# Kernel tuning notes

Measured on AMD Instinct MI355X. Metric: run time of the kernel, lower is better.

The kernel has to match this reference:

```python
import jax, jax.numpy as jnp
import numpy as np

N, E, IN, HID, HEADS, OUT = 20000, 320000, 64, 32, 8, 128
EPS_SM = 1e-16


def setup_inputs() -> dict:
    key = jax.random.key(0)
    ks = iter(jax.random.split(key, 40))
    def g(shape, scale=0.1):
        return jax.random.normal(next(ks), shape, dtype=jnp.float32) * scale
    inp = {
        "x": jax.random.normal(next(ks), (N, IN), dtype=jnp.float32),
        "edge_index": jax.random.randint(next(ks), (2, E), 0, N, dtype=jnp.int64),
        # layer 0: GATConv(64 -> 32, heads=8, concat) => dim 256
        "W0": g((IN, HEADS * HID)), "b0": jnp.zeros((HEADS * HID,), jnp.float32),
        "as0": g((HEADS, HID)), "ad0": g((HEADS, HID)),
        "lng0": jnp.ones((HEADS * HID,), jnp.float32), "lnb0": jnp.zeros((HEADS * HID,), jnp.float32),
        "rW0": g((IN, HEADS * HID)), "rb0": jnp.zeros((HEADS * HID,), jnp.float32),
        "rw0": jnp.ones((1,), jnp.float32),
        # layer 1: GATConv(256 -> 32, heads=8, concat) => dim 256, residual = Identity
        "W1": g((HEADS * HID, HEADS * HID)), "b1": jnp.zeros((HEADS * HID,), jnp.float32),
        "as1": g((HEADS, HID)), "ad1": g((HEADS, HID)),
        "lng1": jnp.ones((HEADS * HID,), jnp.float32), "lnb1": jnp.zeros((HEADS * HID,), jnp.float32),
        "rw1": jnp.ones((1,), jnp.float32),
        # layer 2: GATConv(256 -> 128, heads=8, concat=False mean) => dim 128
        "W2": g((HEADS * HID, HEADS * OUT)), "b2": jnp.zeros((OUT,), jnp.float32),
        "as2": g((HEADS, OUT)), "ad2": g((HEADS, OUT)),
        "lng2": jnp.ones((OUT,), jnp.float32), "lnb2": jnp.zeros((OUT,), jnp.float32),
        "rW2": g((HEADS * HID, OUT)), "rb2": jnp.zeros((OUT,), jnp.float32),
        "rw2": jnp.ones((1,), jnp.float32),
    }
    return inp


def _gat_conv(x, src, dst, W, b, a_s, a_d, heads, out_c, concat):
    n = x.shape[0]
    h = (x @ W).reshape(n, heads, out_c)            # [N,H,C]
    al_s = jnp.sum(h * a_s, axis=-1)                 # [N,H]
    al_d = jnp.sum(h * a_d, axis=-1)
    e = jax.nn.leaky_relu(al_s[src] + al_d[dst], 0.2)  # [E,H]
    m = jax.ops.segment_max(e, dst, num_segments=n)
    m = jnp.where(jnp.isfinite(m), m, 0.0)
    ex = jnp.exp(e - m[dst])
    denom = jax.ops.segment_sum(ex, dst, num_segments=n)
    alpha = ex / (denom[dst] + EPS_SM)               # [E,H]
    msg = alpha[:, :, None] * h[src]                 # [E,H,C]
    out = jax.ops.segment_sum(msg, dst, num_segments=n)  # [N,H,C]
    if concat:
        return out.reshape(n, heads * out_c) + b
    return out.mean(axis=1) + b


def _layer_norm(x, g, b, eps=1e-5):
    mu = x.mean(-1, keepdims=True)
    var = x.var(-1, keepdims=True)
    return (x - mu) * jax.lax.rsqrt(var + eps) * g + b


def reference(x, edge_index, W0, b0, as0, ad0, lng0, lnb0, rW0, rb0, rw0,
              W1, b1, as1, ad1, lng1, lnb1, rw1,
              W2, b2, as2, ad2, lng2, lnb2, rW2, rb2, rw2):
    ei = edge_index.astype(jnp.int32)
    ar = jnp.arange(N, dtype=jnp.int32)
    src = jnp.concatenate([ei[0], ar])               # add self loops
    dst = jnp.concatenate([ei[1], ar])

    # layer 0 (eval mode: dropout is identity)
    g0 = _gat_conv(x, src, dst, W0, b0, as0, ad0, HEADS, HID, True)
    h = _layer_norm(g0, lng0, lnb0) + jax.nn.sigmoid(rw0) * (x @ rW0 + rb0)
    h = jax.nn.elu(h)

    # layer 1 (residual projection = Identity)
    g1 = _gat_conv(h, src, dst, W1, b1, as1, ad1, HEADS, HID, True)
    h = jax.nn.elu(_layer_norm(g1, lng1, lnb1) + jax.nn.sigmoid(rw1) * h)

    # layer 2 (concat=False -> mean over heads)
    g2 = _gat_conv(h, src, dst, W2, b2, as2, ad2, HEADS, OUT, False)
    out = _layer_norm(g2, lng2, lnb2) + jax.nn.sigmoid(rw2) * (h @ rW2 + rb2)
    return out
```

## Files before the change

kernel.cpp:

```cpp
#include <hip/hip_runtime.h>
#include <cstddef>
#include <cstdint>

#define NN 20000
#define EE 320000
#define ET (EE + NN)

typedef __attribute__((ext_vector_type(8))) short bf16x8;
typedef __attribute__((ext_vector_type(4))) float f32x4;

__device__ __forceinline__ unsigned short f2bf_rne(float f) {
  unsigned int u = __float_as_uint(f);
  u += 0x7FFF + ((u >> 16) & 1);
  return (unsigned short)(u >> 16);
}

__device__ __forceinline__ float bf2f(unsigned short b) {
  return __uint_as_float(((unsigned int)b) << 16);
}

__device__ __forceinline__ f32x4 up2(uint2 p) {
  f32x4 v = {__uint_as_float(p.x << 16), __uint_as_float(p.x & 0xFFFF0000u),
             __uint_as_float(p.y << 16), __uint_as_float(p.y & 0xFFFF0000u)};
  return v;
}


__global__ __launch_bounds__(256) void prep_all(
    const float* __restrict__ x, unsigned short* __restrict__ xbf,
    const float* __restrict__ W0, unsigned short* __restrict__ W0T,
    const float* __restrict__ rW0, unsigned short* __restrict__ rW0T,
    const float* __restrict__ W1, unsigned short* __restrict__ W1T,
    const float* __restrict__ rW2, unsigned short* __restrict__ rW2T,
    const float* __restrict__ W2, const float* __restrict__ as2,
    const float* __restrict__ ad2, unsigned short* __restrict__ V16,
    unsigned short* __restrict__ WstkT, int* __restrict__ zbuf, int full) {
  int b = blockIdx.x, t = threadIdx.x;
  if (b < 5000) {
    int i = b * 256 + t;
    if (i < NN * 64) xbf[i] = f2bf_rne(x[i]);
    return;
  }
  b -= 5000;
  if (b < 64) {
    int idx = b * 256 + t, n = idx >> 6, k = idx & 63;
    W0T[idx] = f2bf_rne(W0[(size_t)k * 256 + n]);
    return;
  }
  b -= 64;
  if (b < 64) {
    int idx = b * 256 + t, n = idx >> 6, k = idx & 63;
    rW0T[idx] = f2bf_rne(rW0[(size_t)k * 256 + n]);
    return;
  }
  b -= 64;
  if (b < 256) {
    int idx = b * 256 + t, n = idx >> 8, k = idx & 255;
    W1T[idx] = f2bf_rne(W1[(size_t)k * 256 + n]);
    return;
  }
  b -= 256;
  if (b < 128) {
    int idx = b * 256 + t, n = idx >> 8, k = idx & 255;
    rW2T[idx] = f2bf_rne(rW2[(size_t)k * 128 + n]);
    return;
  }
  b -= 128;
  if (b < 157) {
    int i = b * 256 + t;
    if (i < 2 * NN) zbuf[i] = 0;
    return;
  }
  b -= 157;
  if (!full) return;
  if (b < 16) {
    int r = b, k = t, h = r & 7;
    const float* av = (r < 8) ? (as2 + h * 128) : (ad2 + h * 128);
    const float* wr = W2 + (size_t)k * 1024 + h * 128;
    float v = 0.f;
#pragma unroll 4
    for (int c = 0; c < 128; ++c) v += wr[c] * av[c];
    V16[(size_t)r * 256 + k] = f2bf_rne(v);
    return;
  }
  b -= 16;
  if (b < 128) {
    int c = b, k = t;
#pragma unroll
    for (int h = 0; h < 8; ++h)
      WstkT[(size_t)c * 2048 + h * 256 + k] =
          f2bf_rne(0.125f * W2[(size_t)k * 1024 + h * 128 + c]);
  }
}

#define PREP_BLOCKS (5000 + 64 + 64 + 256 + 128 + 157 + 16 + 128)


__global__ __launch_bounds__(256) void zero_f32(float* __restrict__ p, int n) {
  int i = blockIdx.x * 256 + threadIdx.x;
  if (i < n) p[i] = 0.f;
}

__global__ void tconv(const float* __restrict__ src, unsigned short* __restrict__ dst,
                      int N) {
  int n = blockIdx.x, k = threadIdx.x, K = blockDim.x;
  dst[(size_t)n * K + k] = f2bf_rne(src[(size_t)k * N + n]);
}


__global__ __launch_bounds__(256) void count_kernel(const int* __restrict__ ei,
                                                    int* __restrict__ deg) {
  int e = blockIdx.x * 256 + threadIdx.x;
  if (e < EE) {
    int d = ei[EE + e];
    if (d >= 0 && d < NN) atomicAdd(&deg[d], 1);
  }
}

__global__ __launch_bounds__(1024) void scan_blk(const int* __restrict__ deg,
    int* __restrict__ offs, int* __restrict__ bsum) {
  __shared__ int s[1024];
  int b = blockIdx.x, tid = threadIdx.x;
  int i = b * 1024 + tid;
  s[tid] = (i < NN) ? (deg[i] + 1) : 0;
  __syncthreads();
  for (int off = 1; off < 1024; off <<= 1) {
    int t = (tid >= off) ? s[tid - off] : 0;
    __syncthreads();
    s[tid] += t;
    __syncthreads();
  }
  if (i < NN) offs[i + 1] = s[tid];
  if (tid == 1023) bsum[b] = s[1023];
}

__global__ __launch_bounds__(256) void scan_add(int* __restrict__ offs,
    const int* __restrict__ bsum) {
  int i = blockIdx.x * 256 + threadIdx.x;
  if (i == 0) offs[0] = 0;
  if (i < NN) {
    int b = i >> 10;
    int pre = 0;
    for (int k = 0; k < b; ++k) pre += bsum[k];
    offs[i + 1] += pre;
  }
}

__global__ __launch_bounds__(256) void scatter_kernel(const int* __restrict__ ei,
    const int* __restrict__ offs, int* __restrict__ cursor, int* __restrict__ csr) {
  int e = blockIdx.x * 256 + threadIdx.x;
  if (e >= ET) return;
  int s, d;
  if (e < EE) { s = ei[e]; d = ei[EE + e]; }
  else        { s = e - EE; d = s; }
  if (s < 0 || s >= NN || d < 0 || d >= NN) return;
  int pos = atomicAdd(&cursor[d], 1);
  csr[offs[d] + pos] = s;
}


__global__ __launch_bounds__(256) void gemm_mfma(const unsigned short* __restrict__ A,
    const unsigned short* __restrict__ BT, const float* __restrict__ bias,
    float* __restrict__ C, int M, int K, int ldc) {
  int bm = blockIdx.y * 64, bn = blockIdx.x * 64;
  int tid = threadIdx.x;
  int w = tid >> 6, l = tid & 63;
  int wm = bm + w * 16;
  if (wm >= M) return;
  int lane16 = l & 15, q = l >> 4;
  const unsigned short* ap = A + (size_t)(wm + lane16) * K + q * 8;
  const unsigned short* bp = BT + (size_t)(bn + lane16) * K + q * 8;
  f32x4 acc0 = {0.f, 0.f, 0.f, 0.f}, acc1 = acc0, acc2 = acc0, acc3 = acc0;
#pragma unroll 2
  for (int k0 = 0; k0 < K; k0 += 32) {
    bf16x8 a  = *(const bf16x8*)(ap + k0);
    bf16x8 b0 = *(const bf16x8*)(bp + k0);
    bf16x8 b1 = *(const bf16x8*)(bp + (size_t)16 * K + k0);
    bf16x8 b2 = *(const bf16x8*)(bp + (size_t)32 * K + k0);
    bf16x8 b3 = *(const bf16x8*)(bp + (size_t)48 * K + k0);
    acc0 = __builtin_amdgcn_mfma_f32_16x16x32_bf16(a, b0, acc0, 0, 0, 0);
    acc1 = __builtin_amdgcn_mfma_f32_16x16x32_bf16(a, b1, acc1, 0, 0, 0);
    acc2 = __builtin_amdgcn_mfma_f32_16x16x32_bf16(a, b2, acc2, 0, 0, 0);
    acc3 = __builtin_amdgcn_mfma_f32_16x16x32_bf16(a, b3, acc3, 0, 0, 0);
  }
  int row0 = wm + q * 4;
  int c0 = bn + lane16;
  float bi0 = bias ? bias[c0]      : 0.f;
  float bi1 = bias ? bias[c0 + 16] : 0.f;
  float bi2 = bias ? bias[c0 + 32] : 0.f;
  float bi3 = bias ? bias[c0 + 48] : 0.f;
#pragma unroll
  for (int r = 0; r < 4; ++r) {
    float* crow = C + (size_t)(row0 + r) * ldc;
    crow[c0]      = acc0[r] + bi0;
    crow[c0 + 16] = acc1[r] + bi1;
    crow[c0 + 32] = acc2[r] + bi2;
    crow[c0 + 48] = acc3[r] + bi3;
  }
}

__global__ __launch_bounds__(256) void gemm_l0(const unsigned short* __restrict__ A,
    const unsigned short* __restrict__ W0T, const unsigned short* __restrict__ rW0T,
    const float* __restrict__ rb0, unsigned short* __restrict__ hG,
    unsigned short* __restrict__ resout, const float* __restrict__ as_w,
    const float* __restrict__ ad_w, float* __restrict__ als,
    float* __restrict__ ald, int M) {
  int z = blockIdx.z;
  int bm = blockIdx.y * 64, bn = blockIdx.x * 64;
  int tid = threadIdx.x;
  int w = tid >> 6, l = tid & 63;
  int wm = bm + w * 16;
  if (wm >= M) return;
  int lane16 = l & 15, q = l >> 4;
  const unsigned short* BT = z ? rW0T : W0T;
  const unsigned short* ap = A + (size_t)(wm + lane16) * 64 + q * 8;
  const unsigned short* bp = BT + (size_t)(bn + lane16) * 64 + q * 8;
  f32x4 acc0 = {0.f, 0.f, 0.f, 0.f}, acc1 = acc0, acc2 = acc0, acc3 = acc0;
#pragma unroll
  for (int k0 = 0; k0 < 64; k0 += 32) {
    bf16x8 a  = *(const bf16x8*)(ap + k0);
    bf16x8 b0 = *(const bf16x8*)(bp + k0);
    bf16x8 b1 = *(const bf16x8*)(bp + (size_t)16 * 64 + k0);
    bf16x8 b2 = *(const bf16x8*)(bp + (size_t)32 * 64 + k0);
    bf16x8 b3 = *(const bf16x8*)(bp + (size_t)48 * 64 + k0);
    acc0 = __builtin_amdgcn_mfma_f32_16x16x32_bf16(a, b0, acc0, 0, 0, 0);
    acc1 = __builtin_amdgcn_mfma_f32_16x16x32_bf16(a, b1, acc1, 0, 0, 0);
    acc2 = __builtin_amdgcn_mfma_f32_16x16x32_bf16(a, b2, acc2, 0, 0, 0);
    acc3 = __builtin_amdgcn_mfma_f32_16x16x32_bf16(a, b3, acc3, 0, 0, 0);
  }
  int row0 = wm + q * 4;
  int c0 = bn + lane16;
  if (z == 1) {
    float bi0 = rb0[c0], bi1 = rb0[c0 + 16], bi2 = rb0[c0 + 32], bi3 = rb0[c0 + 48];
#pragma unroll
    for (int r = 0; r < 4; ++r) {
      unsigned short* crow = resout + (size_t)(row0 + r) * 256;
      crow[c0]      = f2bf_rne(acc0[r] + bi0);
      crow[c0 + 16] = f2bf_rne(acc1[r] + bi1);
      crow[c0 + 32] = f2bf_rne(acc2[r] + bi2);
      crow[c0 + 48] = f2bf_rne(acc3[r] + bi3);
    }
    return;
  }
#pragma unroll
  for (int r = 0; r < 4; ++r) {
    unsigned short* crow = hG + (size_t)(row0 + r) * 256;
    crow[c0]      = f2bf_rne(acc0[r]);
    crow[c0 + 16] = f2bf_rne(acc1[r]);
    crow[c0 + 32] = f2bf_rne(acc2[r]);
    crow[c0 + 48] = f2bf_rne(acc3[r]);
  }
  float asA0 = as_w[c0],      asA1 = as_w[c0 + 16];
  float adA0 = ad_w[c0],      adA1 = ad_w[c0 + 16];
  float asB0 = as_w[c0 + 32], asB1 = as_w[c0 + 48];
  float adB0 = ad_w[c0 + 32], adB1 = ad_w[c0 + 48];
  int hA = (bn >> 5), hB = hA + 1;
#pragma unroll
  for (int r = 0; r < 4; ++r) {
    float sA = acc0[r] * asA0 + acc1[r] * asA1;
    float dA = acc0[r] * adA0 + acc1[r] * adA1;
    float sB = acc2[r] * asB0 + acc3[r] * asB1;
    float dB = acc2[r] * adB0 + acc3[r] * adB1;
#pragma unroll
    for (int off = 8; off >= 1; off >>= 1) {
      sA += __shfl_xor(sA, off);
      dA += __shfl_xor(dA, off);
      sB += __shfl_xor(sB, off);
      dB += __shfl_xor(dB, off);
    }
    if (lane16 == 0) {
      int row = row0 + r;
      als[row * 8 + hA] = sA;
      ald[row * 8 + hA] = dA;
      als[row * 8 + hB] = sB;
      ald[row * 8 + hB] = dB;
    }
  }
}

__global__ __launch_bounds__(256) void gemm_mfma_bf_al(const unsigned short* __restrict__ A,
    const unsigned short* __restrict__ BT, unsigned short* __restrict__ C,
    const float* __restrict__ as_w, const float* __restrict__ ad_w,
    float* __restrict__ als, float* __restrict__ ald, int M, int K) {
  int bm = blockIdx.y * 64, bn = blockIdx.x * 64;
  int tid = threadIdx.x;
  int w = tid >> 6, l = tid & 63;
  int wm = bm + w * 16;
  if (wm >= M) return;
  int lane16 = l & 15, q = l >> 4;
  const unsigned short* ap = A + (size_t)(wm + lane16) * K + q * 8;
  const unsigned short* bp = BT + (size_t)(bn + lane16) * K + q * 8;
  f32x4 acc0 = {0.f, 0.f, 0.f, 0.f}, acc1 = acc0, acc2 = acc0, acc3 = acc0;
#pragma unroll 2
  for (int k0 = 0; k0 < K; k0 += 32) {
    bf16x8 a  = *(const bf16x8*)(ap + k0);
    bf16x8 b0 = *(const bf16x8*)(bp + k0);
    bf16x8 b1 = *(const bf16x8*)(bp + (size_t)16 * K + k0);
    bf16x8 b2 = *(const bf16x8*)(bp + (size_t)32 * K + k0);
    bf16x8 b3 = *(const bf16x8*)(bp + (size_t)48 * K + k0);
    acc0 = __builtin_amdgcn_mfma_f32_16x16x32_bf16(a, b0, acc0, 0, 0, 0);
    acc1 = __builtin_amdgcn_mfma_f32_16x16x32_bf16(a, b1, acc1, 0, 0, 0);
    acc2 = __builtin_amdgcn_mfma_f32_16x16x32_bf16(a, b2, acc2, 0, 0, 0);
    acc3 = __builtin_amdgcn_mfma_f32_16x16x32_bf16(a, b3, acc3, 0, 0, 0);
  }
  int row0 = wm + q * 4;
  int c0 = bn + lane16;
#pragma unroll
  for (int r = 0; r < 4; ++r) {
    unsigned short* crow = C + (size_t)(row0 + r) * 256;
    crow[c0]      = f2bf_rne(acc0[r]);
    crow[c0 + 16] = f2bf_rne(acc1[r]);
    crow[c0 + 32] = f2bf_rne(acc2[r]);
    crow[c0 + 48] = f2bf_rne(acc3[r]);
  }
  float asA0 = as_w[c0],      asA1 = as_w[c0 + 16];
  float adA0 = ad_w[c0],      adA1 = ad_w[c0 + 16];
  float asB0 = as_w[c0 + 32], asB1 = as_w[c0 + 48];
  float adB0 = ad_w[c0 + 32], adB1 = ad_w[c0 + 48];
  int hA = (bn >> 5), hB = hA + 1;
#pragma unroll
  for (int r = 0; r < 4; ++r) {
    float sA = acc0[r] * asA0 + acc1[r] * asA1;
    float dA = acc0[r] * adA0 + acc1[r] * adA1;
    float sB = acc2[r] * asB0 + acc3[r] * asB1;
    float dB = acc2[r] * adB0 + acc3[r] * adB1;
#pragma unroll
    for (int off = 8; off >= 1; off >>= 1) {
      sA += __shfl_xor(sA, off);
      dA += __shfl_xor(dA, off);
      sB += __shfl_xor(sB, off);
      dB += __shfl_xor(dB, off);
    }
    if (lane16 == 0) {
      int row = row0 + r;
      als[row * 8 + hA] = sA;
      ald[row * 8 + hA] = dA;
      als[row * 8 + hB] = sB;
      ald[row * 8 + hB] = dB;
    }
  }
}

__global__ __launch_bounds__(256) void gemm_l2a(const unsigned short* __restrict__ A,
    const unsigned short* __restrict__ V16, const unsigned short* __restrict__ rW2T,
    const float* __restrict__ rb2, float* __restrict__ als, float* __restrict__ ald,
    float* __restrict__ res2, int M) {
  int bx = blockIdx.x;
  int bm = blockIdx.y * 64;
  int tid = threadIdx.x;
  int w = tid >> 6, l = tid & 63;
  int wm = bm + w * 16;
  if (wm >= M) return;
  int lane16 = l & 15, q = l >> 4;
  const unsigned short* ap = A + (size_t)(wm + lane16) * 256 + q * 8;
  if (bx == 0) {
    const unsigned short* bp = V16 + (size_t)lane16 * 256 + q * 8;
    f32x4 acc = {0.f, 0.f, 0.f, 0.f};
#pragma unroll
    for (int k0 = 0; k0 < 256; k0 += 32) {
      bf16x8 a = *(const bf16x8*)(ap + k0);
      bf16x8 b = *(const bf16x8*)(bp + k0);
      acc = __builtin_amdgcn_mfma_f32_16x16x32_bf16(a, b, acc, 0, 0, 0);
    }
    int row0 = wm + q * 4;
    float* dst = (lane16 < 8) ? als : ald;
    int h = lane16 & 7;
#pragma unroll
    for (int r = 0; r < 4; ++r)
      dst[(size_t)(row0 + r) * 8 + h] = acc[r];
    return;
  }
  int bn = (bx - 1) * 64;
  const unsigned short* bp = rW2T + (size_t)(bn + lane16) * 256 + q * 8;
  f32x4 acc0 = {0.f, 0.f, 0.f, 0.f}, acc1 = acc0, acc2 = acc0, acc3 = acc0;
#pragma unroll 2
  for (int k0 = 0; k0 < 256; k0 += 32) {
    bf16x8 a  = *(const bf16x8*)(ap + k0);
    bf16x8 b0 = *(const bf16x8*)(bp + k0);
    bf16x8 b1 = *(const bf16x8*)(bp + (size_t)16 * 256 + k0);
    bf16x8 b2 = *(const bf16x8*)(bp + (size_t)32 * 256 + k0);
    bf16x8 b3 = *(const bf16x8*)(bp + (size_t)48 * 256 + k0);
    acc0 = __builtin_amdgcn_mfma_f32_16x16x32_bf16(a, b0, acc0, 0, 0, 0);
    acc1 = __builtin_amdgcn_mfma_f32_16x16x32_bf16(a, b1, acc1, 0, 0, 0);
    acc2 = __builtin_amdgcn_mfma_f32_16x16x32_bf16(a, b2, acc2, 0, 0, 0);
    acc3 = __builtin_amdgcn_mfma_f32_16x16x32_bf16(a, b3, acc3, 0, 0, 0);
  }
  int row0 = wm + q * 4;
  int c0 = bn + lane16;
  float bi0 = rb2[c0], bi1 = rb2[c0 + 16], bi2 = rb2[c0 + 32], bi3 = rb2[c0 + 48];
#pragma unroll
  for (int r = 0; r < 4; ++r) {
    float* crow = res2 + (size_t)(row0 + r) * 128;
    crow[c0]      = acc0[r] + bi0;
    crow[c0 + 16] = acc1[r] + bi1;
    crow[c0 + 32] = acc2[r] + bi2;
    crow[c0 + 48] = acc3[r] + bi3;
  }
}

__global__ __launch_bounds__(256) void gemm_al16(const unsigned short* __restrict__ A,
    const unsigned short* __restrict__ V16, float* __restrict__ als,
    float* __restrict__ ald, int M) {
  int bm = blockIdx.x * 64;
  int tid = threadIdx.x;
  int w = tid >> 6, l = tid & 63;
  int wm = bm + w * 16;
  if (wm >= M) return;
  int lane16 = l & 15, q = l >> 4;
  const unsigned short* ap = A + (size_t)(wm + lane16) * 256 + q * 8;
  const unsigned short* bp = V16 + (size_t)lane16 * 256 + q * 8;
  f32x4 acc = {0.f, 0.f, 0.f, 0.f};
#pragma unroll
  for (int k0 = 0; k0 < 256; k0 += 32) {
    bf16x8 a = *(const bf16x8*)(ap + k0);
    bf16x8 b = *(const bf16x8*)(bp + k0);
    acc = __builtin_amdgcn_mfma_f32_16x16x32_bf16(a, b, acc, 0, 0, 0);
  }
  int row0 = wm + q * 4;
  float* dst = (lane16 < 8) ? als : ald;
  int h = lane16 & 7;
#pragma unroll
  for (int r = 0; r < 4; ++r)
    dst[(size_t)(row0 + r) * 8 + h] = acc[r];
}


__global__ __launch_bounds__(256) void gemm_y_tiled(const unsigned short* __restrict__ A,
    const unsigned short* __restrict__ BT, float* __restrict__ P, int M) {
  __shared__ unsigned short sA[64][72];
  __shared__ unsigned short sB[128][72];
  int bm = blockIdx.x * 64, s = blockIdx.y;
  int tid = threadIdx.x;
  int w = tid >> 6, l = tid & 63;
  int lane16 = l & 15, q = l >> 4;
  int soff = s * 512;
  int r = tid >> 3, c = (tid & 7) * 8;
  int rA0 = min(bm + r, M - 1);
  int rA1 = min(bm + r + 32, M - 1);
  f32x4 acc[8] = {};
#pragma unroll 1
  for (int kt = 0; kt < 8; ++kt) {
    int kb = soff + kt * 64 + c;
    *(bf16x8*)&sA[r][c]      = *(const bf16x8*)(A + (size_t)rA0 * 2048 + kb);
    *(bf16x8*)&sA[r + 32][c] = *(const bf16x8*)(A + (size_t)rA1 * 2048 + kb);
#pragma unroll
    for (int rr = 0; rr < 4; ++rr)
      *(bf16x8*)&sB[r + rr * 32][c] = *(const bf16x8*)(BT + (size_t)(r + rr * 32) * 2048 + kb);
    __syncthreads();
#pragma unroll
    for (int kk = 0; kk < 2; ++kk) {
      bf16x8 a = *(const bf16x8*)&sA[w * 16 + lane16][kk * 32 + q * 8];
#pragma unroll
      for (int t = 0; t < 8; ++t) {
        bf16x8 b = *(const bf16x8*)&sB[t * 16 + lane16][kk * 32 + q * 8];
        acc[t] = __builtin_amdgcn_mfma_f32_16x16x32_bf16(a, b, acc[t], 0, 0, 0);
      }
    }
    __syncthreads();
  }
  int row0 = bm + w * 16 + q * 4;
  float* pbase = P + (size_t)s * ((size_t)M * 128);
#pragma unroll
  for (int r2 = 0; r2 < 4; ++r2) {
    if (row0 + r2 < M) {
      float* prow = pbase + (size_t)(row0 + r2) * 128 + lane16;
#pragma unroll
      for (int t = 0; t < 8; ++t) prow[t * 16] = acc[t][r2];
    }
  }
}


__global__ __launch_bounds__(256) void al2(const float* __restrict__ h,
    const float* __restrict__ aw_s, const float* __restrict__ aw_d,
    float* __restrict__ als, float* __restrict__ ald) {
  int n = blockIdx.x, tid = threadIdx.x;
  int j = tid & 127;
  __shared__ float ss[256], sd[256];
  float v = h[(size_t)n * 256 + tid];
  ss[tid] = v * aw_s[tid];
  sd[tid] = v * aw_d[tid];
  __syncthreads();
  for (int off = 64; off > 0; off >>= 1) {
    if (j < off) { ss[tid] += ss[tid + off]; sd[tid] += sd[tid + off]; }
    __syncthreads();
  }
  if (j == 0) {
    int hh = tid >> 7;
    als[n * 2 + hh] = ss[tid];
    ald[n * 2 + hh] = sd[tid];
  }
}


__global__ __launch_bounds__(256) void agg_epi_w(const unsigned short* __restrict__ hG,
    const float* __restrict__ als, const float* __restrict__ ald,
    const int* __restrict__ offs, const int* __restrict__ csr,
    const float* __restrict__ bias, const float* __restrict__ lng,
    const float* __restrict__ lnb, const unsigned short* __restrict__ resb,
    const float* __restrict__ rw, unsigned short* __restrict__ outbf) {
  int w = threadIdx.x >> 6, l = threadIdx.x & 63;
  int n = blockIdx.x * 4 + w;
  if (n >= NN) return;
  int r0 = offs[n], r1 = offs[n + 1], deg = r1 - r0;
  int h8 = l & 7, e8 = l >> 3, hl = l >> 3;
  float aldn = ald[n * 8 + h8];
  f32x4 acc = {0.f, 0.f, 0.f, 0.f};
  float denacc = 0.f;
  for (int c0 = 0; c0 < deg; c0 += 8) {
    int cn = min(8, deg - c0);
    int src_my = csr[r0 + c0 + min(e8, cn - 1)];
    float ev = als[src_my * 8 + h8] + aldn;
    ev = ev >= 0.f ? ev : 0.2f * ev;
    float aexp = (e8 < cn) ? __expf(ev) : 0.f;
    denacc += aexp;
#pragma unroll 2
    for (int e = 0; e < cn; ++e) {
      int s = __shfl(src_my, e * 8);
      float a = __shfl(aexp, e * 8 + hl);
      uint2 p = *(const uint2*)(hG + (size_t)s * 256 + l * 4);
      acc += a * up2(p);
    }
  }
  denacc += __shfl_xor(denacc, 8);
  denacc += __shfl_xor(denacc, 16);
  denacc += __shfl_xor(denacc, 32);
  float den = __shfl(denacc, hl);
  float dinv = 1.f / (den + 1e-16f);
  float4 bi = ((const float4*)bias)[l];
  uint2 pb = ((const uint2*)resb)[(size_t)n * 64 + l];
  f32x4 rr = up2(pb);
  f32x4 val = {acc.x * dinv + bi.x, acc.y * dinv + bi.y,
               acc.z * dinv + bi.z, acc.w * dinv + bi.w};
  float v1 = val.x + val.y + val.z + val.w;
  float v2 = val.x * val.x + val.y * val.y + val.z * val.z + val.w * val.w;
#pragma unroll
  for (int off = 32; off >= 1; off >>= 1) {
    v1 += __shfl_xor(v1, off);
    v2 += __shfl_xor(v2, off);
  }
  float mu = v1 * (1.f / 256.f);
  float var = v2 * (1.f / 256.f) - mu * mu;
  float rs = rsqrtf(var + 1e-5f);
  float sig = 1.f / (1.f + __expf(-rw[0]));
  float4 lg = ((const float4*)lng)[l];
  float4 lb = ((const float4*)lnb)[l];
  float ov[4];
  const float* valp = (const float*)&val;
  const float* rrp = (const float*)&rr;
  const float* lgp = &lg.x;
  const float* lbp = &lb.x;
#pragma unroll
  for (int k = 0; k < 4; ++k) {
    float rv = (valp[k] - mu) * rs * lgp[k] + lbp[k] + sig * rrp[k];
    ov[k] = rv > 0.f ? rv : (__expf(rv) - 1.f);
  }
  uint2 pk;
  pk.x = (unsigned)f2bf_rne(ov[0]) | ((unsigned)f2bf_rne(ov[1]) << 16);
  pk.y = (unsigned)f2bf_rne(ov[2]) | ((unsigned)f2bf_rne(ov[3]) << 16);
  ((uint2*)outbf)[(size_t)n * 64 + l] = pk;
}


__global__ __launch_bounds__(256) void agg_y_w(const unsigned short* __restrict__ hbf,
    const float* __restrict__ als, const float* __restrict__ ald,
    const int* __restrict__ offs, const int* __restrict__ csr,
    unsigned short* __restrict__ Y) {
  int w = threadIdx.x >> 6, l = threadIdx.x & 63;
  int n = blockIdx.x * 4 + w;
  if (n >= NN) return;
  int r0 = offs[n], r1 = offs[n + 1], deg = r1 - r0;
  int h8 = l & 7, e8 = l >> 3;
  float aldn = ald[n * 8 + h8];
  f32x4 accv[8] = {};
  float denacc = 0.f;
  for (int c0 = 0; c0 < deg; c0 += 8) {
    int cn = min(8, deg - c0);
    int src_my = csr[r0 + c0 + min(e8, cn - 1)];
    float ev = als[src_my * 8 + h8] + aldn;
    ev = ev >= 0.f ? ev : 0.2f * ev;
    float aexp = (e8 < cn) ? __expf(ev) : 0.f;
    denacc += aexp;
    for (int e = 0; e < cn; ++e) {
      int s = __shfl(src_my, e * 8);
      uint2 p = *(const uint2*)(hbf + (size_t)s * 256 + l * 4);
      f32x4 v = up2(p);
#pragma unroll
      for (int h = 0; h < 8; ++h) {
        float a = __shfl(aexp, e * 8 + h);
        accv[h] += a * v;
      }
    }
  }
  denacc += __shfl_xor(denacc, 8);
  denacc += __shfl_xor(denacc, 16);
  denacc += __shfl_xor(denacc, 32);
  unsigned short* yrow = Y + (size_t)n * 2048;
#pragma unroll
  for (int h = 0; h < 8; ++h) {
    float dh = __shfl(denacc, h);
    float sc = 1.f / (dh + 1e-16f);
    f32x4 t = accv[h];
    uint2 pk;
    pk.x = (unsigned)f2bf_rne(t.x * sc) | ((unsigned)f2bf_rne(t.y * sc) << 16);
    pk.y = (unsigned)f2bf_rne(t.z * sc) | ((unsigned)f2bf_rne(t.w * sc) << 16);
    *(uint2*)(yrow + h * 256 + l * 4) = pk;
  }
}


__global__ __launch_bounds__(256) void agg2_pair(const float* __restrict__ h2,
    const float* __restrict__ als, const float* __restrict__ ald,
    const int* __restrict__ offs, const int* __restrict__ csr,
    float* __restrict__ acc_out) {
  int n = blockIdx.x, tid = threadIdx.x;
  int r0 = offs[n], r1 = offs[n + 1];
  __shared__ float s_red[256];
  __shared__ float s_dn[2];
  int hh = tid >> 7, j = tid & 127;
  float aldn = ald[n * 2 + hh];
  float sm = 0.f;
  for (int i = r0 + j; i < r1; i += 128) {
    int s = csr[i];
    float ev = als[s * 2 + hh] + aldn;
    ev = ev >= 0.f ? ev : 0.2f * ev;
    sm += __expf(ev);
  }
  s_red[tid] = sm;
  __syncthreads();
  for (int off = 64; off > 0; off >>= 1) {
    if (j < off) s_red[tid] += s_red[tid + off];
    __syncthreads();
  }
  if (j == 0) s_dn[hh] = s_red[tid] + 1e-16f;
  __syncthreads();
  float dinv = 1.f / s_dn[hh];
  float acc = 0.f;
  for (int i = r0; i < r1; ++i) {
    int s = csr[i];
    float ev = als[s * 2 + hh] + aldn;
    ev = ev >= 0.f ? ev : 0.2f * ev;
    float alpha = __expf(ev) * dinv;
    acc += alpha * h2[(size_t)s * 256 + tid];
  }
  s_red[tid] = acc;
  __syncthreads();
  if (tid < 128)
    acc_out[(size_t)n * 128 + tid] += 0.125f * (s_red[tid] + s_red[tid + 128]);
}


__global__ __launch_bounds__(128) void epi_out_res4(const float* __restrict__ P,
    const float* __restrict__ b2, const float* __restrict__ lng,
    const float* __restrict__ lnb, const float* __restrict__ res2,
    const float* __restrict__ rw, float* __restrict__ out) {
  int n = blockIdx.x, tid = threadIdx.x;
  __shared__ float sw1[2], sw2[2];
  size_t stride = (size_t)NN * 128;
  size_t idx = (size_t)n * 128 + tid;
  float g = P[idx] + P[stride + idx] + P[2 * stride + idx] + P[3 * stride + idx] + b2[tid];
  float v1 = g, v2 = g * g;
#pragma unroll
  for (int off = 32; off >= 1; off >>= 1) {
    v1 += __shfl_xor(v1, off);
    v2 += __shfl_xor(v2, off);
  }
  if ((tid & 63) == 0) { sw1[tid >> 6] = v1; sw2[tid >> 6] = v2; }
  __syncthreads();
  float tot1 = sw1[0] + sw1[1], tot2 = sw2[0] + sw2[1];
  float mu = tot1 * (1.f / 128.f);
  float var = tot2 * (1.f / 128.f) - mu * mu;
  float rs = rsqrtf(var + 1e-5f);
  float sig = 1.f / (1.f + __expf(-rw[0]));
  out[idx] = (g - mu) * rs * lng[tid] + lnb[tid] + sig * res2[idx];
}

__global__ __launch_bounds__(128) void epi_out_res(float* __restrict__ acc,
    const float* __restrict__ b2, const float* __restrict__ lng,
    const float* __restrict__ lnb, const float* __restrict__ res2,
    const float* __restrict__ rw) {
  int n = blockIdx.x, tid = threadIdx.x;
  __shared__ float s1[128], s2[128];
  __shared__ float s_mu, s_rs;
  float g = acc[(size_t)n * 128 + tid] + b2[tid];
  s1[tid] = g; s2[tid] = g * g;
  __syncthreads();
  for (int off = 64; off > 0; off >>= 1) {
    if (tid < off) { s1[tid] += s1[tid + off]; s2[tid] += s2[tid + off]; }
    __syncthreads();
  }
  if (tid == 0) {
    float mu = s1[0] * (1.f / 128.f);
    float var = s2[0] * (1.f / 128.f) - mu * mu;
    s_mu = mu; s_rs = rsqrtf(var + 1e-5f);
  }
  __syncthreads();
  float sig = 1.f / (1.f + __expf(-rw[0]));
  float lnv = (g - s_mu) * s_rs * lng[tid] + lnb[tid];
  acc[(size_t)n * 128 + tid] = lnv + sig * res2[(size_t)n * 128 + tid];
}

__global__ __launch_bounds__(128) void epi_out_mv(float* __restrict__ acc,
    const float* __restrict__ b2, const float* __restrict__ lng,
    const float* __restrict__ lnb, const unsigned short* __restrict__ hB,
    const float* __restrict__ rW2, const float* __restrict__ rb2,
    const float* __restrict__ rw) {
  int n = blockIdx.x, tid = threadIdx.x;
  __shared__ float srow[256];
  __shared__ float s1[128], s2[128];
  __shared__ float s_mu, s_rs;
  srow[tid] = bf2f(hB[(size_t)n * 256 + tid]);
  srow[tid + 128] = bf2f(hB[(size_t)n * 256 + tid + 128]);
  float g = acc[(size_t)n * 128 + tid] + b2[tid];
  s1[tid] = g; s2[tid] = g * g;
  __syncthreads();
  for (int off = 64; off > 0; off >>= 1) {
    if (tid < off) { s1[tid] += s1[tid + off]; s2[tid] += s2[tid + off]; }
    __syncthreads();
  }
  if (tid == 0) {
    float mu = s1[0] * (1.f / 128.f);
    float var = s2[0] * (1.f / 128.f) - mu * mu;
    s_mu = mu; s_rs = rsqrtf(var + 1e-5f);
  }
  __syncthreads();
  float rv = rb2[tid];
#pragma unroll 4
  for (int k = 0; k < 256; ++k) rv += srow[k] * rW2[(size_t)k * 128 + tid];
  float sig = 1.f / (1.f + __expf(-rw[0]));
  float lnv = (g - s_mu) * s_rs * lng[tid] + lnb[tid];
  acc[(size_t)n * 128 + tid] = lnv + sig * rv;
}


extern "C" void kernel_launch(void* const* d_in, const int* in_sizes, int n_in,
                              void* d_out, int out_size, void* d_ws, size_t ws_size,
                              hipStream_t stream) {
  const float* x   = (const float*)d_in[0];
  const int*   ei  = (const int*)d_in[1];
  const float* W0  = (const float*)d_in[2];
  const float* b0  = (const float*)d_in[3];
  const float* as0 = (const float*)d_in[4];
  const float* ad0 = (const float*)d_in[5];
  const float* lng0= (const float*)d_in[6];
  const float* lnb0= (const float*)d_in[7];
  const float* rW0 = (const float*)d_in[8];
  const float* rb0 = (const float*)d_in[9];
  const float* rw0 = (const float*)d_in[10];
  const float* W1  = (const float*)d_in[11];
  const float* b1  = (const float*)d_in[12];
  const float* as1 = (const float*)d_in[13];
  const float* ad1 = (const float*)d_in[14];
  const float* lng1= (const float*)d_in[15];
  const float* lnb1= (const float*)d_in[16];
  const float* rw1 = (const float*)d_in[17];
  const float* W2  = (const float*)d_in[18];
  const float* b2  = (const float*)d_in[19];
  const float* as2 = (const float*)d_in[20];
  const float* ad2 = (const float*)d_in[21];
  const float* lng2= (const float*)d_in[22];
  const float* lnb2= (const float*)d_in[23];
  const float* rW2 = (const float*)d_in[24];
  const float* rb2 = (const float*)d_in[25];
  const float* rw2 = (const float*)d_in[26];
  float* outp = (float*)d_out;

  char* w = (char*)d_ws;
  auto carve = [&](size_t bytes) -> char* {
    char* p = w;
    w += (bytes + 255) & ~(size_t)255;
    return p;
  };
  float* bufH = (float*)carve((size_t)NN * 256 * 4);
  float* bufR = (float*)carve((size_t)NN * 256 * 4);
  float* als  = (float*)carve((size_t)NN * 8 * 4);
  float* ald  = (float*)carve((size_t)NN * 8 * 4);
  int* deg    = (int*)carve((size_t)2 * NN * 4);
  int* cursor = deg + NN;
  int* offs   = (int*)carve((size_t)(NN + 1) * 4);
  int* bsum   = (int*)carve((size_t)32 * 4);
  int* csr    = (int*)carve((size_t)ET * 4);
  unsigned short* xbf  = (unsigned short*)carve((size_t)NN * 64 * 2);
  unsigned short* hbf0 = (unsigned short*)carve((size_t)NN * 256 * 2);
  unsigned short* hbf1 = (unsigned short*)carve((size_t)NN * 256 * 2);
  unsigned short* W0T  = (unsigned short*)carve((size_t)256 * 64 * 2);
  unsigned short* rW0T = (unsigned short*)carve((size_t)256 * 64 * 2);
  unsigned short* W1T  = (unsigned short*)carve((size_t)256 * 256 * 2);
  unsigned short* W2T  = (unsigned short*)carve((size_t)1024 * 256 * 2);
  unsigned short* rW2T = (unsigned short*)carve((size_t)128 * 256 * 2);
  size_t base = (size_t)(w - (char*)d_ws);
  if (ws_size < base) return;
  unsigned short* hG = (unsigned short*)bufH;

  size_t full_extra = (((size_t)16 * 256 * 2 + 255) & ~(size_t)255)
                    + (((size_t)128 * 2048 * 2 + 255) & ~(size_t)255)
                    + (((size_t)NN * 2048 * 2 + 255) & ~(size_t)255);
  size_t res2_extra = (((size_t)NN * 128 * 4 + 255) & ~(size_t)255);
  bool full = (ws_size - base) >= full_extra;
  unsigned short *V16 = nullptr, *WstkT = nullptr, *Ybuf = nullptr;
  if (full) {
    V16   = (unsigned short*)carve((size_t)16 * 256 * 2);
    WstkT = (unsigned short*)carve((size_t)128 * 2048 * 2);
    Ybuf  = (unsigned short*)carve((size_t)NN * 2048 * 2);
  }
  float* res2 = nullptr;
  if ((ws_size - (size_t)(w - (char*)d_ws)) >= res2_extra)
    res2 = (float*)carve((size_t)NN * 128 * 4);

  prep_all<<<PREP_BLOCKS, 256, 0, stream>>>(x, xbf, W0, W0T, rW0, rW0T, W1, W1T,
                                            rW2, rW2T, W2, as2, ad2, V16, WstkT,
                                            deg, full ? 1 : 0);
  if (!full) tconv<<<1024, 256, 0, stream>>>(W2, W2T, 1024);

  count_kernel<<<(EE + 255) / 256, 256, 0, stream>>>(ei, deg);
  int nb = (NN + 1023) / 1024;
  scan_blk<<<nb, 1024, 0, stream>>>(deg, offs, bsum);
  scan_add<<<(NN + 255) / 256, 256, 0, stream>>>(offs, bsum);
  scatter_kernel<<<(ET + 255) / 256, 256, 0, stream>>>(ei, offs, cursor, csr);

  dim3 g256(4, (NN + 63) / 64);
  dim3 g128(2, (NN + 63) / 64);
  int gagg = (NN + 3) / 4;

  gemm_l0<<<dim3(4, (NN + 63) / 64, 2), 256, 0, stream>>>(
      xbf, W0T, rW0T, rb0, hG, hbf1, as0, ad0, als, ald, NN);
  agg_epi_w<<<gagg, 256, 0, stream>>>(hG, als, ald, offs, csr, b0, lng0,
                                      lnb0, hbf1, rw0, hbf0);

  gemm_mfma_bf_al<<<g256, 256, 0, stream>>>(hbf0, W1T, hG, as1, ad1, als, ald, NN, 256);
  agg_epi_w<<<gagg, 256, 0, stream>>>(hG, als, ald, offs, csr, b1, lng1,
                                      lnb1, hbf0, rw1, hbf1);

  if (full && res2) {
    gemm_l2a<<<dim3(3, (NN + 63) / 64), 256, 0, stream>>>(hbf1, V16, rW2T, rb2,
                                                          als, ald, res2, NN);
    agg_y_w<<<gagg, 256, 0, stream>>>(hbf1, als, ald, offs, csr, Ybuf);
    float* partial = bufH;
    gemm_y_tiled<<<dim3((NN + 63) / 64, 4), 256, 0, stream>>>(Ybuf, WstkT,
                                                              partial, NN);
    epi_out_res4<<<NN, 128, 0, stream>>>(partial, b2, lng2, lnb2, res2, rw2, outp);
  } else if (full) {
    gemm_al16<<<(NN + 63) / 64, 256, 0, stream>>>(hbf1, V16, als, ald, NN);
    agg_y_w<<<gagg, 256, 0, stream>>>(hbf1, als, ald, offs, csr, Ybuf);
    gemm_mfma<<<g128, 256, 0, stream>>>(Ybuf, WstkT, nullptr, outp, NN, 2048, 128);
    epi_out_mv<<<NN, 128, 0, stream>>>(outp, b2, lng2, lnb2, hbf1, rW2, rb2, rw2);
  } else {
    if (res2)
      gemm_mfma<<<g128, 256, 0, stream>>>(hbf1, rW2T, rb2, res2, NN, 256, 128);
    zero_f32<<<(NN * 128 + 255) / 256, 256, 0, stream>>>(outp, NN * 128);
    for (int p = 0; p < 4; ++p) {
      gemm_mfma<<<g256, 256, 0, stream>>>(hbf1, W2T + (size_t)p * 256 * 256, nullptr,
                                          bufH, NN, 256, 256);
      al2<<<NN, 256, 0, stream>>>(bufH, as2 + p * 256, ad2 + p * 256, als, ald);
      agg2_pair<<<NN, 256, 0, stream>>>(bufH, als, ald, offs, csr, outp);
    }
    if (res2)
      epi_out_res<<<NN, 128, 0, stream>>>(outp, b2, lng2, lnb2, res2, rw2);
    else
      epi_out_mv<<<NN, 128, 0, stream>>>(outp, b2, lng2, lnb2, hbf1, rW2, rb2, rw2);
  }
}
```

Baseline: 393.4 us.

## Fuse final layer-norm epilogue into split-K GEMM via last-block counter

Removes the separate epi_out_res4 launch. Each 64-row tile of the split-K GEMM bumps an atomic counter after writing its partial, and the fourth block to finish sums the four partials and applies bias, layer norm and the scaled residual in place. The Y buffer layout is also switched to head-interleaved (k*8+h), so agg_y_w writes one 16-byte packed store per channel group instead of eight 8-byte stores. The weight-stacking prep is updated to match, and the zeroed buffer is extended to cover the 313 counters. In exchange it relies on threadfence-and-atomic ordering, and the epilogue runs on only a quarter of the blocks.

```diff
diff --git a/kernel.cpp b/kernel.cpp
--- a/kernel.cpp
+++ b/kernel.cpp
@@ -66,12 +66,12 @@
     return;
   }
   b -= 128;
-  if (b < 157) {
+  if (b < 158) {
     int i = b * 256 + t;
-    if (i < 2 * NN) zbuf[i] = 0;
+    if (i < 2 * NN + 320) zbuf[i] = 0;
     return;
   }
-  b -= 157;
+  b -= 158;
   if (!full) return;
   if (b < 16) {
     int r = b, k = t, h = r & 7;
@@ -88,12 +88,12 @@
     int c = b, k = t;
 #pragma unroll
     for (int h = 0; h < 8; ++h)
-      WstkT[(size_t)c * 2048 + h * 256 + k] =
+      WstkT[(size_t)c * 2048 + k * 8 + h] =
           f2bf_rne(0.125f * W2[(size_t)k * 1024 + h * 128 + c]);
   }
 }
 
-#define PREP_BLOCKS (5000 + 64 + 64 + 256 + 128 + 157 + 16 + 128)
+#define PREP_BLOCKS (5000 + 64 + 64 + 256 + 128 + 158 + 16 + 128)
 
 
 __global__ __launch_bounds__(256) void zero_f32(float* __restrict__ p, int n) {
@@ -426,9 +426,14 @@
 
 
 __global__ __launch_bounds__(256) void gemm_y_tiled(const unsigned short* __restrict__ A,
-    const unsigned short* __restrict__ BT, float* __restrict__ P, int M) {
+    const unsigned short* __restrict__ BT, float* __restrict__ P, int M,
+    int* __restrict__ cnt, const float* __restrict__ b2,
+    const float* __restrict__ lng, const float* __restrict__ lnb,
+    const float* __restrict__ res2, const float* __restrict__ rw,
+    float* __restrict__ out) {
   __shared__ unsigned short sA[64][72];
   __shared__ unsigned short sB[128][72];
+  __shared__ int s_last;
   int bm = blockIdx.x * 64, s = blockIdx.y;
   int tid = threadIdx.x;
   int w = tid >> 6, l = tid & 63;
@@ -467,6 +472,33 @@
 #pragma unroll
       for (int t = 0; t < 8; ++t) prow[t * 16] = acc[t][r2];
     }
+  }
+  __threadfence();
+  __syncthreads();
+  if (tid == 0) s_last = (atomicAdd(&cnt[blockIdx.x], 1) == 3);
+  __syncthreads();
+  if (!s_last) return;
+  size_t stride = (size_t)M * 128;
+  float sig = 1.f / (1.f + __expf(-rw[0]));
+  for (int rr = w; rr < 64; rr += 4) {
+    int row = bm + rr;
+    if (row >= M) continue;
+    size_t idx = (size_t)row * 128 + l;
+    float g0 = P[idx] + P[stride + idx] + P[2 * stride + idx] + P[3 * stride + idx]
+             + b2[l];
+    float g1 = P[idx + 64] + P[stride + idx + 64] + P[2 * stride + idx + 64]
+             + P[3 * stride + idx + 64] + b2[l + 64];
+    float v1 = g0 + g1, v2 = g0 * g0 + g1 * g1;
+#pragma unroll
+    for (int off = 32; off >= 1; off >>= 1) {
+      v1 += __shfl_xor(v1, off);
+      v2 += __shfl_xor(v2, off);
+    }
+    float mu = v1 * (1.f / 128.f);
+    float var = v2 * (1.f / 128.f) - mu * mu;
+    float rs = rsqrtf(var + 1e-5f);
+    out[idx]      = (g0 - mu) * rs * lng[l] + lnb[l] + sig * res2[idx];
+    out[idx + 64] = (g1 - mu) * rs * lng[l + 64] + lnb[l + 64] + sig * res2[idx + 64];
   }
 }
 
@@ -595,16 +627,19 @@
   denacc += __shfl_xor(denacc, 8);
   denacc += __shfl_xor(denacc, 16);
   denacc += __shfl_xor(denacc, 32);
-  unsigned short* yrow = Y + (size_t)n * 2048;
-#pragma unroll
-  for (int h = 0; h < 8; ++h) {
-    float dh = __shfl(denacc, h);
-    float sc = 1.f / (dh + 1e-16f);
-    f32x4 t = accv[h];
-    uint2 pk;
-    pk.x = (unsigned)f2bf_rne(t.x * sc) | ((unsigned)f2bf_rne(t.y * sc) << 16);
-    pk.y = (unsigned)f2bf_rne(t.z * sc) | ((unsigned)f2bf_rne(t.w * sc) << 16);
-    *(uint2*)(yrow + h * 256 + l * 4) = pk;
+  float sc[8];
+#pragma unroll
+  for (int h = 0; h < 8; ++h)
+    sc[h] = 1.f / (__shfl(denacc, h) + 1e-16f);
+  unsigned short* yrow = Y + (size_t)n * 2048 + l * 32;
+#pragma unroll
+  for (int j = 0; j < 4; ++j) {
+    uint4 pk;
+    pk.x = (unsigned)f2bf_rne(accv[0][j] * sc[0]) | ((unsigned)f2bf_rne(accv[1][j] * sc[1]) << 16);
+    pk.y = (unsigned)f2bf_rne(accv[2][j] * sc[2]) | ((unsigned)f2bf_rne(accv[3][j] * sc[3]) << 16);
+    pk.z = (unsigned)f2bf_rne(accv[4][j] * sc[4]) | ((unsigned)f2bf_rne(accv[5][j] * sc[5]) << 16);
+    pk.w = (unsigned)f2bf_rne(accv[6][j] * sc[6]) | ((unsigned)f2bf_rne(accv[7][j] * sc[7]) << 16);
+    *(uint4*)(yrow + j * 8) = pk;
   }
 }
 
@@ -649,31 +684,6 @@
     acc_out[(size_t)n * 128 + tid] += 0.125f * (s_red[tid] + s_red[tid + 128]);
 }
 
-
-__global__ __launch_bounds__(128) void epi_out_res4(const float* __restrict__ P,
-    const float* __restrict__ b2, const float* __restrict__ lng,
-    const float* __restrict__ lnb, const float* __restrict__ res2,
-    const float* __restrict__ rw, float* __restrict__ out) {
-  int n = blockIdx.x, tid = threadIdx.x;
-  __shared__ float sw1[2], sw2[2];
-  size_t stride = (size_t)NN * 128;
-  size_t idx = (size_t)n * 128 + tid;
-  float g = P[idx] + P[stride + idx] + P[2 * stride + idx] + P[3 * stride + idx] + b2[tid];
-  float v1 = g, v2 = g * g;
-#pragma unroll
-  for (int off = 32; off >= 1; off >>= 1) {
-    v1 += __shfl_xor(v1, off);
-    v2 += __shfl_xor(v2, off);
-  }
-  if ((tid & 63) == 0) { sw1[tid >> 6] = v1; sw2[tid >> 6] = v2; }
-  __syncthreads();
-  float tot1 = sw1[0] + sw1[1], tot2 = sw2[0] + sw2[1];
-  float mu = tot1 * (1.f / 128.f);
-  float var = tot2 * (1.f / 128.f) - mu * mu;
-  float rs = rsqrtf(var + 1e-5f);
-  float sig = 1.f / (1.f + __expf(-rw[0]));
-  out[idx] = (g - mu) * rs * lng[tid] + lnb[tid] + sig * res2[idx];
-}
 
 __global__ __launch_bounds__(128) void epi_out_res(float* __restrict__ acc,
     const float* __restrict__ b2, const float* __restrict__ lng,
@@ -775,8 +785,9 @@
   float* bufR = (float*)carve((size_t)NN * 256 * 4);
   float* als  = (float*)carve((size_t)NN * 8 * 4);
   float* ald  = (float*)carve((size_t)NN * 8 * 4);
-  int* deg    = (int*)carve((size_t)2 * NN * 4);
+  int* deg    = (int*)carve((size_t)(2 * NN + 320) * 4);
   int* cursor = deg + NN;
+  int* cnt    = deg + 2 * NN;
   int* offs   = (int*)carve((size_t)(NN + 1) * 4);
   int* bsum   = (int*)carve((size_t)32 * 4);
   int* csr    = (int*)carve((size_t)ET * 4);
@@ -836,9 +847,8 @@
                                                           als, ald, res2, NN);
     agg_y_w<<<gagg, 256, 0, stream>>>(hbf1, als, ald, offs, csr, Ybuf);
     float* partial = bufH;
-    gemm_y_tiled<<<dim3((NN + 63) / 64, 4), 256, 0, stream>>>(Ybuf, WstkT,
-                                                              partial, NN);
-    epi_out_res4<<<NN, 128, 0, stream>>>(partial, b2, lng2, lnb2, res2, rw2, outp);
+    gemm_y_tiled<<<dim3((NN + 63) / 64, 4), 256, 0, stream>>>(
+        Ybuf, WstkT, partial, NN, cnt, b2, lng2, lnb2, res2, rw2, outp);
   } else if (full) {
     gemm_al16<<<(NN + 63) / 64, 256, 0, stream>>>(hbf1, V16, als, ald, NN);
     agg_y_w<<<gagg, 256, 0, stream>>>(hbf1, als, ald, offs, csr, Ybuf);
```

Result: slower. 564.1 us (+43.4%).
